# Kernel optimization log

Measured on AMD Instinct MI355X. Metric: run time of the kernel, lower is better.

The kernel has to match this reference:

```python
import jax, jax.numpy as jnp
import numpy as np

NUM_CLASSES = 128  # fixed stand-in for len(torch.unique(targets))
B, N_SUP, N_QRY, D = 16, 4096, 4096, 512


def setup_inputs() -> dict:
    key = jax.random.key(0)
    k1, k2, k3, k4 = jax.random.split(key, 4)
    return {
        "support_embeddings": jax.random.normal(k1, (B, N_SUP, D), dtype=jnp.float32),
        "query_embeddings": jax.random.normal(k2, (B, N_QRY, D), dtype=jnp.float32),
        "support_targets": jax.random.randint(k3, (B, N_SUP), 0, NUM_CLASSES),
        "query_targets": jax.random.randint(k4, (B, N_QRY), 0, NUM_CLASSES),
    }


def _prototypes(emb, tgt):
    # emb: (N, D), tgt: (N,) -> (C, D) class means (scatter-add + count clamp)
    sums = jax.ops.segment_sum(emb, tgt, num_segments=NUM_CLASSES)
    cnt = jax.ops.segment_sum(jnp.ones(tgt.shape, emb.dtype), tgt, num_segments=NUM_CLASSES)
    return sums / jnp.maximum(cnt, 1.0)[:, None]


def reference(support_embeddings, query_embeddings, support_targets, query_targets):
    protos = jax.vmap(_prototypes)(support_embeddings, support_targets)  # (B, C, D)
    # squared euclidean distances (B, C, Nq) via ||p||^2 + ||q||^2 - 2 p.q (GEMM form)
    p_sq = jnp.sum(protos * protos, axis=-1)                      # (B, C)
    q_sq = jnp.sum(query_embeddings * query_embeddings, axis=-1)  # (B, Nq)
    cross = jnp.einsum('bcd,bqd->bcq', protos, query_embeddings)  # (B, C, Nq)
    dist = p_sq[:, :, None] + q_sq[:, None, :] - 2.0 * cross
    predictions = jnp.argmin(dist, axis=1)                        # (B, Nq)
    # F.cross_entropy(-dist, targets): class dim is axis 1
    logp = jax.nn.log_softmax(-dist, axis=1)                      # (B, C, Nq)
    nll = -jnp.take_along_axis(logp, query_targets[:, None, :], axis=1)[:, 0, :]
    loss = jnp.mean(nll)
    accuracy = jnp.mean((predictions == query_targets).astype(jnp.float32))
    return predictions, loss, accuracy
```

## Files before the change

### kernel.cpp

```cpp
#include <hip/hip_runtime.h>
#include <math.h>

#define B_ 16
#define NSUP_ 4096
#define NQ_ 4096
#define D_ 512
#define C_ 128
#define MARGIN 0.02f

typedef __attribute__((ext_vector_type(8))) short bf16x8;
typedef __attribute__((ext_vector_type(4))) float f32x4;

__device__ inline short f2bf(float f) {
    unsigned u = __float_as_uint(f);
    unsigned r = (u + 0x7fffu + ((u >> 16) & 1u)) >> 16;
    return (short)r;
}
__device__ inline float bf2f(short h) {
    return __uint_as_float(((unsigned)(unsigned short)h) << 16);
}

__global__ __launch_bounds__(256) void sort_kernel(
    const int* __restrict__ tgt, int* __restrict__ perm,
    int* __restrict__ class_base, int* __restrict__ class_cnt,
    int* __restrict__ flag_count, int* __restrict__ acc_delta)
{
    __shared__ int cnt[C_];
    __shared__ int base[C_];
    int b = blockIdx.x, tid = threadIdx.x;
    if (tid < C_) cnt[tid] = 0;
    __syncthreads();
    for (int i = tid; i < NSUP_; i += 256) atomicAdd(&cnt[tgt[b * NSUP_ + i]], 1);
    __syncthreads();
    if (tid == 0) { int s = 0; for (int c = 0; c < C_; c++) { base[c] = s; s += cnt[c]; } }
    __syncthreads();
    if (tid < C_) {
        class_base[b * C_ + tid] = base[tid];
        class_cnt [b * C_ + tid] = cnt[tid];
    }
    if (b == 0 && tid == 0) { *flag_count = 0; *acc_delta = 0; }
    __syncthreads();
    for (int i = tid; i < NSUP_; i += 256) {
        int c = tgt[b * NSUP_ + i];
        int pos = atomicAdd(&base[c], 1);
        perm[b * NSUP_ + pos] = i;
    }
}

__global__ __launch_bounds__(256) void proto_kernel(
    const float* __restrict__ sup, const int* __restrict__ class_base,
    const int* __restrict__ class_cnt, const int* __restrict__ perm,
    float* __restrict__ pf32, double* __restrict__ p64,
    double* __restrict__ psq64, float* __restrict__ psq32)
{
    __shared__ int rows[256];
    __shared__ double red[256];
    int g = blockIdx.x, b = g >> 7, c = g & 127;
    int tid = threadIdx.x;
    int base = class_base[b * C_ + c], cnt = class_cnt[b * C_ + c];
    const float* eb = sup + (size_t)b * NSUP_ * D_;
    int d = 2 * tid;
    double a0 = 0.0, a1 = 0.0;
    for (int r0 = 0; r0 < cnt; r0 += 256) {
        int nr = min(256, cnt - r0);
        __syncthreads();
        if (tid < nr) rows[tid] = perm[b * NSUP_ + base + r0 + tid];
        __syncthreads();
        for (int r = 0; r < nr; r++) {
            float2 v = *(const float2*)(eb + (size_t)rows[r] * D_ + d);
            a0 += (double)v.x; a1 += (double)v.y;
        }
    }
    double cw = (double)(cnt > 1 ? cnt : 1);
    a0 /= cw; a1 /= cw;
    size_t ob = (size_t)(b * C_ + c) * D_ + d;
    pf32[ob] = (float)a0; pf32[ob + 1] = (float)a1;
    p64[ob] = a0; p64[ob + 1] = a1;
    red[tid] = a0 * a0 + a1 * a1;
    __syncthreads();
    for (int s = 128; s > 0; s >>= 1) {
        if (tid < s) red[tid] += red[tid + s];
        __syncthreads();
    }
    if (tid == 0) { psq64[g] = red[0]; psq32[g] = (float)red[0]; }
}

__global__ __launch_bounds__(256) void screen_kernel(
    const float* __restrict__ qry, const int* __restrict__ qtgt,
    const float* __restrict__ pf32, const float* __restrict__ psq32,
    float* __restrict__ out_pred, double* __restrict__ blk_loss,
    float* __restrict__ blk_acc, int* __restrict__ flags, int* __restrict__ flag_count)
{
    __shared__ __align__(16) short Ah[C_ * 64];
    __shared__ __align__(16) short Al[C_ * 64];
    __shared__ __align__(16) short Bh[128 * 64];
    __shared__ __align__(16) short Bl[128 * 64];
    __shared__ float ldsPsq[C_];
    __shared__ double wl[4];
    __shared__ float  wa[4];

    int blk = blockIdx.x;
    int b   = blk >> 5;
    int qb  = (blk & 31) * 128;
    int tid = threadIdx.x;
    int wave = tid >> 6, lane = tid & 63;
    int quad = lane >> 4, n16 = lane & 15;

    if (tid < C_) ldsPsq[tid] = psq32[b * C_ + tid];

    f32x4 acc[8][2];
    #pragma unroll
    for (int mt = 0; mt < 8; mt++)
        #pragma unroll
        for (int nt = 0; nt < 2; nt++)
            acc[mt][nt] = (f32x4){0.f, 0.f, 0.f, 0.f};

    const float* pb = pf32 + (size_t)b * C_ * D_;
    const float* qbB = qry + ((size_t)b * NQ_ + qb) * D_;

    for (int ch = 0; ch < 8; ch++) {
        __syncthreads();
        #pragma unroll
        for (int it = 0; it < 4; it++) {
            int t2 = tid + 256 * it;
            int c = t2 >> 3, grp = t2 & 7;
            const float* src = pb + (size_t)c * D_ + ch * 64 + grp * 8;
            float4 f0 = *(const float4*)(src);
            float4 f1 = *(const float4*)(src + 4);
            float xv[8] = {f0.x, f0.y, f0.z, f0.w, f1.x, f1.y, f1.z, f1.w};
            bf16x8 h8, l8;
            #pragma unroll
            for (int e = 0; e < 8; e++) {
                short hb = f2bf(xv[e]);
                h8[e] = hb;
                l8[e] = f2bf(xv[e] - bf2f(hb));
            }
            int tile2 = ((c >> 4) << 1) + (grp >> 2);
            int lp = ((grp & 3) << 4) + (c & 15);
            int addr = (tile2 * 64 + lp) * 8;
            *(bf16x8*)&Ah[addr] = h8;
            *(bf16x8*)&Al[addr] = l8;
        }
        #pragma unroll
        for (int it = 0; it < 4; it++) {
            int t2 = tid + 256 * it;
            int q = t2 >> 3, grp = t2 & 7;
            const float* src = qbB + (size_t)q * D_ + ch * 64 + grp * 8;
            float4 f0 = *(const float4*)(src);
            float4 f1 = *(const float4*)(src + 4);
            float xv[8] = {f0.x, f0.y, f0.z, f0.w, f1.x, f1.y, f1.z, f1.w};
            bf16x8 h8, l8;
            #pragma unroll
            for (int e = 0; e < 8; e++) {
                short hb = f2bf(xv[e]);
                h8[e] = hb;
                l8[e] = f2bf(xv[e] - bf2f(hb));
            }
            int tile2 = ((q >> 4) << 1) + (grp >> 2);
            int lp = ((grp & 3) << 4) + (q & 15);
            int addr = (tile2 * 64 + lp) * 8;
            *(bf16x8*)&Bh[addr] = h8;
            *(bf16x8*)&Bl[addr] = l8;
        }
        __syncthreads();

        int nt0 = wave * 2, nt1 = wave * 2 + 1;
        #pragma unroll
        for (int ks = 0; ks < 2; ks++) {
            bf16x8 bh0 = *(const bf16x8*)&Bh[((nt0 * 2 + ks) * 64 + lane) * 8];
            bf16x8 bl0 = *(const bf16x8*)&Bl[((nt0 * 2 + ks) * 64 + lane) * 8];
            bf16x8 bh1 = *(const bf16x8*)&Bh[((nt1 * 2 + ks) * 64 + lane) * 8];
            bf16x8 bl1 = *(const bf16x8*)&Bl[((nt1 * 2 + ks) * 64 + lane) * 8];
            #pragma unroll
            for (int mt = 0; mt < 8; mt++) {
                bf16x8 ah = *(const bf16x8*)&Ah[((mt * 2 + ks) * 64 + lane) * 8];
                bf16x8 al = *(const bf16x8*)&Al[((mt * 2 + ks) * 64 + lane) * 8];
                acc[mt][0] = __builtin_amdgcn_mfma_f32_16x16x32_bf16(ah, bh0, acc[mt][0], 0, 0, 0);
                acc[mt][0] = __builtin_amdgcn_mfma_f32_16x16x32_bf16(ah, bl0, acc[mt][0], 0, 0, 0);
                acc[mt][0] = __builtin_amdgcn_mfma_f32_16x16x32_bf16(al, bh0, acc[mt][0], 0, 0, 0);
                acc[mt][1] = __builtin_amdgcn_mfma_f32_16x16x32_bf16(ah, bh1, acc[mt][1], 0, 0, 0);
                acc[mt][1] = __builtin_amdgcn_mfma_f32_16x16x32_bf16(ah, bl1, acc[mt][1], 0, 0, 0);
                acc[mt][1] = __builtin_amdgcn_mfma_f32_16x16x32_bf16(al, bh1, acc[mt][1], 0, 0, 0);
            }
        }
    }

    float4 psqv[8];
    #pragma unroll
    for (int mt = 0; mt < 8; mt++)
        psqv[mt] = *(const float4*)&ldsPsq[mt * 16 + quad * 4];

    double wloss = 0.0; float wacc = 0.0f;

    #pragma unroll
    for (int nt = 0; nt < 2; nt++) {
        int ntg = wave * 2 + nt;
        int qloc = ntg * 16 + n16;
        int gq = b * NQ_ + qb + qloc;
        int tq = qtgt[gq];

        float b1 = 1e30f, b2 = 1e30f, dt = 1e30f, lm = -1e30f;
        int c1 = 0;
        #pragma unroll
        for (int mt = 0; mt < 8; mt++) {
            #pragma unroll
            for (int r = 0; r < 4; r++) {
                float d = psqv[mt][r] - 2.0f * acc[mt][nt][r];
                int c = mt * 16 + quad * 4 + r;
                if (d < b1) { b2 = b1; b1 = d; c1 = c; }
                else if (d < b2) { b2 = d; }
                lm = fmaxf(lm, -d);
                if (c == tq) dt = d;
            }
        }
        float ls = 0.0f;
        #pragma unroll
        for (int mt = 0; mt < 8; mt++) {
            #pragma unroll
            for (int r = 0; r < 4; r++) {
                float d = psqv[mt][r] - 2.0f * acc[mt][nt][r];
                ls += __expf(-d - lm);
            }
        }
        #pragma unroll
        for (int off = 16; off <= 32; off <<= 1) {
            float o1 = __shfl_xor(b1, off, 64);
            int   oc = __shfl_xor(c1, off, 64);
            float o2 = __shfl_xor(b2, off, 64);
            float n2 = fminf(fmaxf(b1, o1), fminf(b2, o2));
            if (o1 < b1 || (o1 == b1 && oc < c1)) { b1 = o1; c1 = oc; }
            b2 = n2;
            float om = __shfl_xor(lm, off, 64);
            float os = __shfl_xor(ls, off, 64);
            float nm = fmaxf(lm, om);
            ls = ls * __expf(lm - nm) + os * __expf(om - nm);
            lm = nm;
            dt = fminf(dt, __shfl_xor(dt, off, 64));
        }
        if (quad == 0) {
            wloss += (double)(dt + lm) + (double)logf(ls);
            wacc  += (c1 == tq) ? 1.0f : 0.0f;
            out_pred[gq] = (float)c1;
            if (b2 - b1 < MARGIN) {
                int pos = atomicAdd(flag_count, 1);
                flags[pos] = gq;
            }
        }
    }

    #pragma unroll
    for (int off = 1; off <= 8; off <<= 1) {
        wloss += __shfl_xor(wloss, off, 64);
        wacc  += __shfl_xor(wacc,  off, 64);
    }
    if (lane == 0) { wl[wave] = wloss; wa[wave] = wacc; }
    __syncthreads();
    if (tid == 0) {
        blk_loss[blk] = wl[0] + wl[1] + wl[2] + wl[3];
        blk_acc[blk]  = wa[0] + wa[1] + wa[2] + wa[3];
    }
}

__global__ __launch_bounds__(256) void rescue_kernel(
    const float* __restrict__ qry, const int* __restrict__ qtgt,
    const double* __restrict__ p64, const double* __restrict__ psq64,
    const int* __restrict__ flags, const int* __restrict__ flag_count,
    float* __restrict__ out_pred, int* __restrict__ acc_delta)
{
    int tid = threadIdx.x, wave = tid >> 6, lane = tid & 63;
    int cnt = *flag_count;
    for (int f = blockIdx.x * 4 + wave; f < cnt; f += 1024) {
        int gq = flags[f];
        int b  = gq >> 12;
        const float* qp = qry + (size_t)gq * D_;
        float4 qa = *(const float4*)(qp + 8 * lane);
        float4 qb4 = *(const float4*)(qp + 8 * lane + 4);
        double q[8] = {(double)qa.x,(double)qa.y,(double)qa.z,(double)qa.w,
                       (double)qb4.x,(double)qb4.y,(double)qb4.z,(double)qb4.w};
        double qsq = 0.0;
        #pragma unroll
        for (int k = 0; k < 8; k++) qsq = fma(q[k], q[k], qsq);
        for (int off = 32; off; off >>= 1) qsq += __shfl_xor(qsq, off, 64);

        const double* pb = p64 + (size_t)b * C_ * D_;
        double bd = 1e300; int bc = 0;
        for (int c = 0; c < C_; c += 2) {
            const double* pr0 = pb + (size_t)c * D_ + 8 * lane;
            const double* pr1 = pr0 + D_;
            double dot0 = 0.0, dot1 = 0.0;
            #pragma unroll
            for (int k = 0; k < 8; k++) {
                dot0 = fma(pr0[k], q[k], dot0);
                dot1 = fma(pr1[k], q[k], dot1);
            }
            for (int off = 32; off; off >>= 1) {
                dot0 += __shfl_xor(dot0, off, 64);
                dot1 += __shfl_xor(dot1, off, 64);
            }
            double d0 = psq64[b * C_ + c]     + qsq - 2.0 * dot0;
            double d1 = psq64[b * C_ + c + 1] + qsq - 2.0 * dot1;
            if (d0 < bd) { bd = d0; bc = c; }
            if (d1 < bd) { bd = d1; bc = c + 1; }
        }
        if (lane == 0) {
            int tq = qtgt[gq];
            int oldc = (int)out_pred[gq];
            if (oldc != bc) {
                out_pred[gq] = (float)bc;
                int delta = ((bc == tq) ? 1 : 0) - ((oldc == tq) ? 1 : 0);
                if (delta) atomicAdd(acc_delta, delta);
            }
        }
    }
}

__global__ __launch_bounds__(256) void finalize_kernel(
    const double* __restrict__ blk_loss, const float* __restrict__ blk_acc,
    const int* __restrict__ acc_delta, float* __restrict__ out)
{
    __shared__ double rl[256];
    __shared__ float  ra[256];
    int tid = threadIdx.x;
    double s = 0.0; float a = 0.0f;
    for (int i = tid; i < 512; i += 256) { s += blk_loss[i]; a += blk_acc[i]; }
    rl[tid] = s; ra[tid] = a;
    __syncthreads();
    for (int st = 128; st; st >>= 1) {
        if (tid < st) { rl[tid] += rl[tid + st]; ra[tid] += ra[tid + st]; }
        __syncthreads();
    }
    if (tid == 0) {
        out[B_*NQ_    ] = (float)(rl[0] / (double)(B_ * NQ_));
        out[B_*NQ_ + 1] = (ra[0] + (float)(*acc_delta)) / (float)(B_ * NQ_);
    }
}

extern "C" void kernel_launch(void* const* d_in, const int* in_sizes, int n_in,
                              void* d_out, int out_size, void* d_ws, size_t ws_size,
                              hipStream_t stream) {
    const float* sup  = (const float*)d_in[0];
    const float* qry  = (const float*)d_in[1];
    const int*   stgt = (const int*)d_in[2];
    const int*   qtgt = (const int*)d_in[3];
    float* out = (float*)d_out;

    char* ws = (char*)d_ws;
    constexpr size_t O_P64   = 0;
    constexpr size_t O_PF32  = O_P64   + 8388608;
    constexpr size_t O_PSQ64 = O_PF32  + 4194304;
    constexpr size_t O_PSQ32 = O_PSQ64 + 16384;
    constexpr size_t O_CBASE = O_PSQ32 + 8192;
    constexpr size_t O_CCNT  = O_CBASE + 8192;
    constexpr size_t O_PERM  = O_CCNT  + 8192;
    constexpr size_t O_BLOSS = O_PERM  + 262144;
    constexpr size_t O_BACC  = O_BLOSS + 4096;
    constexpr size_t O_FLAGS = O_BACC  + 2048;
    constexpr size_t O_CNT   = O_FLAGS + 262144;

    double* p64       = (double*)(ws + O_P64);
    float*  pf32      = (float*) (ws + O_PF32);
    double* psq64     = (double*)(ws + O_PSQ64);
    float*  psq32     = (float*) (ws + O_PSQ32);
    int*    cbase     = (int*)   (ws + O_CBASE);
    int*    ccnt      = (int*)   (ws + O_CCNT);
    int*    perm      = (int*)   (ws + O_PERM);
    double* blk_loss  = (double*)(ws + O_BLOSS);
    float*  blk_acc   = (float*) (ws + O_BACC);
    int*    flags     = (int*)   (ws + O_FLAGS);
    int*    flag_count= (int*)   (ws + O_CNT);
    int*    acc_delta = flag_count + 1;

    hipLaunchKernelGGL(sort_kernel,   dim3(16),   dim3(256), 0, stream,
                       stgt, perm, cbase, ccnt, flag_count, acc_delta);
    hipLaunchKernelGGL(proto_kernel,  dim3(2048), dim3(256), 0, stream,
                       sup, cbase, ccnt, perm, pf32, p64, psq64, psq32);
    hipLaunchKernelGGL(screen_kernel, dim3(512),  dim3(256), 0, stream,
                       qry, qtgt, pf32, psq32, out, blk_loss, blk_acc, flags, flag_count);
    hipLaunchKernelGGL(rescue_kernel, dim3(256),  dim3(256), 0, stream,
                       qry, qtgt, p64, psq64, flags, flag_count, out, acc_delta);
    hipLaunchKernelGGL(finalize_kernel, dim3(1),  dim3(256), 0, stream,
                       blk_loss, blk_acc, acc_delta, out);
}
```

Measured before the change: 396.5 us.

## Pre-split prototypes to bf16 tiles and double-buffer screen kernel loads

```diff
diff --git a/kernel.cpp b/kernel.cpp
--- a/kernel.cpp
+++ b/kernel.cpp
@@ -18,6 +18,20 @@
 }
 __device__ inline float bf2f(short h) {
     return __uint_as_float(((unsigned)(unsigned short)h) << 16);
+}
+__device__ inline void gload16(const void* g, void* l) {
+    __builtin_amdgcn_global_load_lds(
+        (const __attribute__((address_space(1))) void*)g,
+        (__attribute__((address_space(3))) void*)l, 16, 0, 0);
+}
+__device__ inline void conv8(const float4& fa, const float4& fb, bf16x8& h8, bf16x8& l8) {
+    float xv[8] = {fa.x, fa.y, fa.z, fa.w, fb.x, fb.y, fb.z, fb.w};
+    #pragma unroll
+    for (int e = 0; e < 8; e++) {
+        short hb = f2bf(xv[e]);
+        h8[e] = hb;
+        l8[e] = f2bf(xv[e] - bf2f(hb));
+    }
 }
 
 __global__ __launch_bounds__(256) void sort_kernel(
@@ -50,51 +64,79 @@
 __global__ __launch_bounds__(256) void proto_kernel(
     const float* __restrict__ sup, const int* __restrict__ class_base,
     const int* __restrict__ class_cnt, const int* __restrict__ perm,
-    float* __restrict__ pf32, double* __restrict__ p64,
-    double* __restrict__ psq64, float* __restrict__ psq32)
+    short* __restrict__ Ahg, short* __restrict__ Alg,
+    double* __restrict__ p64, double* __restrict__ psq64, float* __restrict__ psq32)
 {
     __shared__ int rows[256];
-    __shared__ double red[256];
+    __shared__ double sums[2][512];
+    __shared__ float pm[512];
+    __shared__ double red[128];
     int g = blockIdx.x, b = g >> 7, c = g & 127;
     int tid = threadIdx.x;
+    int half = tid >> 7, d0 = (tid & 127) * 4;
     int base = class_base[b * C_ + c], cnt = class_cnt[b * C_ + c];
     const float* eb = sup + (size_t)b * NSUP_ * D_;
-    int d = 2 * tid;
-    double a0 = 0.0, a1 = 0.0;
+    double a0 = 0.0, a1 = 0.0, a2 = 0.0, a3 = 0.0;
     for (int r0 = 0; r0 < cnt; r0 += 256) {
         int nr = min(256, cnt - r0);
         __syncthreads();
         if (tid < nr) rows[tid] = perm[b * NSUP_ + base + r0 + tid];
         __syncthreads();
-        for (int r = 0; r < nr; r++) {
-            float2 v = *(const float2*)(eb + (size_t)rows[r] * D_ + d);
-            a0 += (double)v.x; a1 += (double)v.y;
-        }
-    }
+        for (int r = half; r < nr; r += 2) {
+            float4 v = *(const float4*)(eb + (size_t)rows[r] * D_ + d0);
+            a0 += (double)v.x; a1 += (double)v.y; a2 += (double)v.z; a3 += (double)v.w;
+        }
+    }
+    sums[half][d0 + 0] = a0; sums[half][d0 + 1] = a1;
+    sums[half][d0 + 2] = a2; sums[half][d0 + 3] = a3;
+    __syncthreads();
     double cw = (double)(cnt > 1 ? cnt : 1);
-    a0 /= cw; a1 /= cw;
-    size_t ob = (size_t)(b * C_ + c) * D_ + d;
-    pf32[ob] = (float)a0; pf32[ob + 1] = (float)a1;
-    p64[ob] = a0; p64[ob + 1] = a1;
-    red[tid] = a0 * a0 + a1 * a1;
-    __syncthreads();
-    for (int s = 128; s > 0; s >>= 1) {
+    if (tid < 128) {
+        double ps = 0.0;
+        size_t ob = (size_t)(b * C_ + c) * D_ + d0;
+        #pragma unroll
+        for (int j = 0; j < 4; j++) {
+            double m = (sums[0][d0 + j] + sums[1][d0 + j]) / cw;
+            p64[ob + j] = m;
+            pm[d0 + j] = (float)m;
+            ps += m * m;
+        }
+        red[tid] = ps;
+    }
+    __syncthreads();
+    for (int s = 64; s > 0; s >>= 1) {
         if (tid < s) red[tid] += red[tid + s];
         __syncthreads();
     }
     if (tid == 0) { psq64[g] = red[0]; psq32[g] = (float)red[0]; }
+    if (tid < 64) {
+        int ch = tid >> 2, ktile = tid & 3;
+        int mt = c >> 4;
+        bf16x8 h8, l8;
+        #pragma unroll
+        for (int e = 0; e < 8; e++) {
+            float x = pm[tid * 8 + e];
+            short hb = f2bf(x);
+            h8[e] = hb;
+            l8[e] = f2bf(x - bf2f(hb));
+        }
+        size_t goff = ((((size_t)b * 16 + ch) * 8 + mt) * 64 + ktile * 16 + (c & 15));
+        *(bf16x8*)(Ahg + goff * 8) = h8;
+        *(bf16x8*)(Alg + goff * 8) = l8;
+    }
 }
 
 __global__ __launch_bounds__(256) void screen_kernel(
     const float* __restrict__ qry, const int* __restrict__ qtgt,
-    const float* __restrict__ pf32, const float* __restrict__ psq32,
+    const short* __restrict__ Ahg, const short* __restrict__ Alg,
+    const float* __restrict__ psq32,
     float* __restrict__ out_pred, double* __restrict__ blk_loss,
     float* __restrict__ blk_acc, int* __restrict__ flags, int* __restrict__ flag_count)
 {
-    __shared__ __align__(16) short Ah[C_ * 64];
-    __shared__ __align__(16) short Al[C_ * 64];
-    __shared__ __align__(16) short Bh[128 * 64];
-    __shared__ __align__(16) short Bl[128 * 64];
+    __shared__ __align__(16) short Ah[2][4096];
+    __shared__ __align__(16) short Al[2][4096];
+    __shared__ __align__(16) short Bh[2][4096];
+    __shared__ __align__(16) short Bl[2][4096];
     __shared__ float ldsPsq[C_];
     __shared__ double wl[4];
     __shared__ float  wa[4];
@@ -115,74 +157,91 @@
         for (int nt = 0; nt < 2; nt++)
             acc[mt][nt] = (f32x4){0.f, 0.f, 0.f, 0.f};
 
-    const float* pb = pf32 + (size_t)b * C_ * D_;
     const float* qbB = qry + ((size_t)b * NQ_ + qb) * D_;
-
-    for (int ch = 0; ch < 8; ch++) {
+    const short* AhB = Ahg + (size_t)b * 16 * 4096;
+    const short* AlB = Alg + (size_t)b * 16 * 4096;
+
+    const int G0 = tid, G1 = tid + 256;
+    const float* bsrc0 = qbB + (size_t)(((G0 >> 6) << 4) + (G0 & 15)) * D_ + (((G0 >> 4) & 3) << 3);
+    const float* bsrc1 = qbB + (size_t)(((G1 >> 6) << 4) + (G1 & 15)) * D_ + (((G1 >> 4) & 3) << 3);
+
+    float4 bq0a, bq0b, bq1a, bq1b;
+
+    bq0a = *(const float4*)(bsrc0);
+    bq0b = *(const float4*)(bsrc0 + 4);
+    bq1a = *(const float4*)(bsrc1);
+    bq1b = *(const float4*)(bsrc1 + 4);
+    {
+        char* dh = (char*)&Ah[0][0];
+        char* dl = (char*)&Al[0][0];
+        gload16(AhB + tid * 8,        dh + tid * 16);
+        gload16(AhB + 2048 + tid * 8, dh + 4096 + tid * 16);
+        gload16(AlB + tid * 8,        dl + tid * 16);
+        gload16(AlB + 2048 + tid * 8, dl + 4096 + tid * 16);
+    }
+    {
+        bf16x8 h8, l8;
+        conv8(bq0a, bq0b, h8, l8);
+        *(bf16x8*)&Bh[0][G0 * 8] = h8;
+        *(bf16x8*)&Bl[0][G0 * 8] = l8;
+    }
+    {
+        bf16x8 h8, l8;
+        conv8(bq1a, bq1b, h8, l8);
+        *(bf16x8*)&Bh[0][G1 * 8] = h8;
+        *(bf16x8*)&Bl[0][G1 * 8] = l8;
+    }
+    __syncthreads();
+
+    #pragma unroll 2
+    for (int ch = 0; ch < 16; ch++) {
+        int p = ch & 1;
+        if (ch < 15) {
+            int cn = ch + 1;
+            bq0a = *(const float4*)(bsrc0 + cn * 32);
+            bq0b = *(const float4*)(bsrc0 + cn * 32 + 4);
+            bq1a = *(const float4*)(bsrc1 + cn * 32);
+            bq1b = *(const float4*)(bsrc1 + cn * 32 + 4);
+            const short* sh = AhB + cn * 4096;
+            const short* sl = AlB + cn * 4096;
+            char* dh = (char*)&Ah[p ^ 1][0];
+            char* dl = (char*)&Al[p ^ 1][0];
+            gload16(sh + tid * 8,        dh + tid * 16);
+            gload16(sh + 2048 + tid * 8, dh + 4096 + tid * 16);
+            gload16(sl + tid * 8,        dl + tid * 16);
+            gload16(sl + 2048 + tid * 8, dl + 4096 + tid * 16);
+        }
+        int nt0 = wave * 2, nt1 = nt0 + 1;
+        bf16x8 bh0 = *(const bf16x8*)&Bh[p][(nt0 * 64 + lane) * 8];
+        bf16x8 bl0 = *(const bf16x8*)&Bl[p][(nt0 * 64 + lane) * 8];
+        bf16x8 bh1 = *(const bf16x8*)&Bh[p][(nt1 * 64 + lane) * 8];
+        bf16x8 bl1 = *(const bf16x8*)&Bl[p][(nt1 * 64 + lane) * 8];
+        #pragma unroll
+        for (int mt = 0; mt < 8; mt++) {
+            bf16x8 ah = *(const bf16x8*)&Ah[p][(mt * 64 + lane) * 8];
+            bf16x8 al = *(const bf16x8*)&Al[p][(mt * 64 + lane) * 8];
+            acc[mt][0] = __builtin_amdgcn_mfma_f32_16x16x32_bf16(ah, bh0, acc[mt][0], 0, 0, 0);
+            acc[mt][0] = __builtin_amdgcn_mfma_f32_16x16x32_bf16(ah, bl0, acc[mt][0], 0, 0, 0);
+            acc[mt][0] = __builtin_amdgcn_mfma_f32_16x16x32_bf16(al, bh0, acc[mt][0], 0, 0, 0);
+            acc[mt][1] = __builtin_amdgcn_mfma_f32_16x16x32_bf16(ah, bh1, acc[mt][1], 0, 0, 0);
+            acc[mt][1] = __builtin_amdgcn_mfma_f32_16x16x32_bf16(ah, bl1, acc[mt][1], 0, 0, 0);
+            acc[mt][1] = __builtin_amdgcn_mfma_f32_16x16x32_bf16(al, bh1, acc[mt][1], 0, 0, 0);
+        }
+        if (ch < 15) {
+            {
+                bf16x8 h8, l8;
+                conv8(bq0a, bq0b, h8, l8);
+                *(bf16x8*)&Bh[p ^ 1][G0 * 8] = h8;
+                *(bf16x8*)&Bl[p ^ 1][G0 * 8] = l8;
+            }
+            {
+                bf16x8 h8, l8;
+                conv8(bq1a, bq1b, h8, l8);
+                *(bf16x8*)&Bh[p ^ 1][G1 * 8] = h8;
+                *(bf16x8*)&Bl[p ^ 1][G1 * 8] = l8;
+            }
+        }
         __syncthreads();
-        #pragma unroll
-        for (int it = 0; it < 4; it++) {
-            int t2 = tid + 256 * it;
-            int c = t2 >> 3, grp = t2 & 7;
-            const float* src = pb + (size_t)c * D_ + ch * 64 + grp * 8;
-            float4 f0 = *(const float4*)(src);
-            float4 f1 = *(const float4*)(src + 4);
-            float xv[8] = {f0.x, f0.y, f0.z, f0.w, f1.x, f1.y, f1.z, f1.w};
-            bf16x8 h8, l8;
-            #pragma unroll
-            for (int e = 0; e < 8; e++) {
-                short hb = f2bf(xv[e]);
-                h8[e] = hb;
-                l8[e] = f2bf(xv[e] - bf2f(hb));
-            }
-            int tile2 = ((c >> 4) << 1) + (grp >> 2);
-            int lp = ((grp & 3) << 4) + (c & 15);
-            int addr = (tile2 * 64 + lp) * 8;
-            *(bf16x8*)&Ah[addr] = h8;
-            *(bf16x8*)&Al[addr] = l8;
-        }
-        #pragma unroll
-        for (int it = 0; it < 4; it++) {
-            int t2 = tid + 256 * it;
-            int q = t2 >> 3, grp = t2 & 7;
-            const float* src = qbB + (size_t)q * D_ + ch * 64 + grp * 8;
-            float4 f0 = *(const float4*)(src);
-            float4 f1 = *(const float4*)(src + 4);
-            float xv[8] = {f0.x, f0.y, f0.z, f0.w, f1.x, f1.y, f1.z, f1.w};
-            bf16x8 h8, l8;
-            #pragma unroll
-            for (int e = 0; e < 8; e++) {
-                short hb = f2bf(xv[e]);
-                h8[e] = hb;
-                l8[e] = f2bf(xv[e] - bf2f(hb));
-            }
-            int tile2 = ((q >> 4) << 1) + (grp >> 2);
-            int lp = ((grp & 3) << 4) + (q & 15);
-            int addr = (tile2 * 64 + lp) * 8;
-            *(bf16x8*)&Bh[addr] = h8;
-            *(bf16x8*)&Bl[addr] = l8;
-        }
-        __syncthreads();
-
-        int nt0 = wave * 2, nt1 = wave * 2 + 1;
-        #pragma unroll
-        for (int ks = 0; ks < 2; ks++) {
-            bf16x8 bh0 = *(const bf16x8*)&Bh[((nt0 * 2 + ks) * 64 + lane) * 8];
-            bf16x8 bl0 = *(const bf16x8*)&Bl[((nt0 * 2 + ks) * 64 + lane) * 8];
-            bf16x8 bh1 = *(const bf16x8*)&Bh[((nt1 * 2 + ks) * 64 + lane) * 8];
-            bf16x8 bl1 = *(const bf16x8*)&Bl[((nt1 * 2 + ks) * 64 + lane) * 8];
-            #pragma unroll
-            for (int mt = 0; mt < 8; mt++) {
-                bf16x8 ah = *(const bf16x8*)&Ah[((mt * 2 + ks) * 64 + lane) * 8];
-                bf16x8 al = *(const bf16x8*)&Al[((mt * 2 + ks) * 64 + lane) * 8];
-                acc[mt][0] = __builtin_amdgcn_mfma_f32_16x16x32_bf16(ah, bh0, acc[mt][0], 0, 0, 0);
-                acc[mt][0] = __builtin_amdgcn_mfma_f32_16x16x32_bf16(ah, bl0, acc[mt][0], 0, 0, 0);
-                acc[mt][0] = __builtin_amdgcn_mfma_f32_16x16x32_bf16(al, bh0, acc[mt][0], 0, 0, 0);
-                acc[mt][1] = __builtin_amdgcn_mfma_f32_16x16x32_bf16(ah, bh1, acc[mt][1], 0, 0, 0);
-                acc[mt][1] = __builtin_amdgcn_mfma_f32_16x16x32_bf16(ah, bl1, acc[mt][1], 0, 0, 0);
-                acc[mt][1] = __builtin_amdgcn_mfma_f32_16x16x32_bf16(al, bh1, acc[mt][1], 0, 0, 0);
-            }
-        }
     }
 
     float4 psqv[8];
@@ -346,8 +405,9 @@
 
     char* ws = (char*)d_ws;
     constexpr size_t O_P64   = 0;
-    constexpr size_t O_PF32  = O_P64   + 8388608;
-    constexpr size_t O_PSQ64 = O_PF32  + 4194304;
+    constexpr size_t O_AH    = O_P64   + 8388608;
+    constexpr size_t O_AL    = O_AH    + 2097152;
+    constexpr size_t O_PSQ64 = O_AL    + 2097152;
     constexpr size_t O_PSQ32 = O_PSQ64 + 16384;
     constexpr size_t O_CBASE = O_PSQ32 + 8192;
     constexpr size_t O_CCNT  = O_CBASE + 8192;
@@ -358,7 +418,8 @@
     constexpr size_t O_CNT   = O_FLAGS + 262144;
 
     double* p64       = (double*)(ws + O_P64);
-    float*  pf32      = (float*) (ws + O_PF32);
+    short*  Ahg       = (short*) (ws + O_AH);
+    short*  Alg       = (short*) (ws + O_AL);
     double* psq64     = (double*)(ws + O_PSQ64);
     float*  psq32     = (float*) (ws + O_PSQ32);
     int*    cbase     = (int*)   (ws + O_CBASE);
@@ -373,9 +434,9 @@
     hipLaunchKernelGGL(sort_kernel,   dim3(16),   dim3(256), 0, stream,
                        stgt, perm, cbase, ccnt, flag_count, acc_delta);
     hipLaunchKernelGGL(proto_kernel,  dim3(2048), dim3(256), 0, stream,
-                       sup, cbase, ccnt, perm, pf32, p64, psq64, psq32);
+                       sup, cbase, ccnt, perm, Ahg, Alg, p64, psq64, psq32);
     hipLaunchKernelGGL(screen_kernel, dim3(512),  dim3(256), 0, stream,
-                       qry, qtgt, pf32, psq32, out, blk_loss, blk_acc, flags, flag_count);
+                       qry, qtgt, Ahg, Alg, psq32, out, blk_loss, blk_acc, flags, flag_count);
     hipLaunchKernelGGL(rescue_kernel, dim3(256),  dim3(256), 0, stream,
                        qry, qtgt, p64, psq64, flags, flag_count, out, acc_delta);
     hipLaunchKernelGGL(finalize_kernel, dim3(1),  dim3(256), 0, stream,
```

Measured after the change: 382.8 us. 1.04x faster.
